# Kernel optimization log

Hardware: AMD Instinct MI355X
Metric: run time of the kernel (lower is better)

## Reference

```python
import jax, jax.numpy as jnp
import numpy as np

N_QUBITS = 8
N_LAYERS = 3
BATCH = 8192


def setup_inputs() -> dict:
    key = jax.random.key(0)
    k0, k1, k2, k3 = jax.random.split(key, 4)
    return {
        "x": jax.random.normal(k0, (BATCH, N_QUBITS), jnp.float32),
        "quantum_weights": jax.random.normal(k1, (N_LAYERS, N_QUBITS, 2), jnp.float32) * 0.1,
        "W1": jax.random.normal(k2, (N_QUBITS, 64), jnp.float32) / np.float32(np.sqrt(N_QUBITS)),
        "b1": jnp.zeros((64,), jnp.float32),
        "W2": jax.random.normal(k3, (64, 256), jnp.float32) / np.float32(np.sqrt(64)),
        "b2": jnp.zeros((256,), jnp.float32),
    }


def _ry(theta):
    # RY(t) = [[cos t/2, -sin t/2], [sin t/2, cos t/2]]; theta: [] or [B]
    c = jnp.cos(theta * 0.5)
    s = jnp.sin(theta * 0.5)
    U = jnp.stack([jnp.stack([c, -s], axis=-1), jnp.stack([s, c], axis=-1)], axis=-2)
    return U.astype(jnp.complex64)


def _rz(theta):
    # RZ(t) = diag(e^{-it/2}, e^{it/2})
    em = jnp.exp(-0.5j * theta.astype(jnp.complex64))
    ep = jnp.exp(0.5j * theta.astype(jnp.complex64))
    z = jnp.zeros_like(em)
    return jnp.stack([jnp.stack([em, z], axis=-1), jnp.stack([z, ep], axis=-1)], axis=-2)


def _apply_1q(state, U, q):
    # state: [B, 2,2,...,2]; qubit q lives on axis q+1. U: [2,2] (shared) or [B,2,2].
    s = jnp.moveaxis(state, q + 1, -1)
    if U.ndim == 3:
        s = jnp.einsum('b...i,bji->b...j', s, U)
    else:
        s = jnp.einsum('b...i,ji->b...j', s, U)
    return jnp.moveaxis(s, -1, q + 1)


def _cnot(state, c, t):
    # flip target bit on the control=1 slice
    s = jnp.moveaxis(state, (c + 1, t + 1), (1, 2))
    s = jnp.stack([s[:, 0], s[:, 1, ::-1]], axis=1)
    return jnp.moveaxis(s, (1, 2), (c + 1, t + 1))


def _quantum_forward(x, qw):
    B = x.shape[0]
    xmin = x.min(axis=1, keepdims=True)
    xmax = x.max(axis=1, keepdims=True)
    xn = (x - xmin) / (xmax - xmin + 1e-8)
    # |0...0> state, shape [B, 2]*n
    state = jnp.zeros((B,) + (2,) * N_QUBITS, jnp.complex64)
    state = state.at[(slice(None),) + (0,) * N_QUBITS].set(1.0)
    # feature encoding: RY(x_norm * pi), per-sample angles
    for q in range(N_QUBITS):
        state = _apply_1q(state, _ry(xn[:, q] * jnp.pi), q)
    # variational layers
    for layer in range(N_LAYERS):
        for q in range(N_QUBITS):
            state = _apply_1q(state, _ry(qw[layer, q, 0]), q)
            state = _apply_1q(state, _rz(qw[layer, q, 1]), q)
        for q in range(N_QUBITS):
            state = _cnot(state, q, (q + 1) % N_QUBITS)
    probs = jnp.real(state * jnp.conj(state))  # [B, 2]*n, float32
    z = []
    for q in range(N_QUBITS):
        p = probs.sum(axis=tuple(a for a in range(1, N_QUBITS + 1) if a != q + 1))
        z.append(p[:, 0] - p[:, 1])  # <Z_q>
    return jnp.stack(z, axis=1)  # [B, n_qubits]


def reference(x, quantum_weights, W1, b1, W2, b2):
    z = _quantum_forward(x, quantum_weights).astype(jnp.float32)
    h = jax.nn.relu(z @ W1 + b1)
    return h @ W2 + b2
```

## Files before the change

### kernel.cpp

```cpp
#include <hip/hip_runtime.h>

#define NQ 8
#define NLAYERS 3

typedef unsigned int uint2ev __attribute__((ext_vector_type(2)));

template<int MASK>
__device__ __forceinline__ float xorlane(float v, int r) {
    if constexpr (MASK == 1) {
        return __int_as_float(__builtin_amdgcn_mov_dpp(__float_as_int(v), 0xB1, 0xF, 0xF, false));
    } else if constexpr (MASK == 2) {
        return __int_as_float(__builtin_amdgcn_mov_dpp(__float_as_int(v), 0x4E, 0xF, 0xF, false));
    } else if constexpr (MASK == 4) {
        float a = __int_as_float(__builtin_amdgcn_update_dpp(0, __float_as_int(v), 0x114, 0xF, 0xF, false));
        float b = __int_as_float(__builtin_amdgcn_update_dpp(0, __float_as_int(v), 0x104, 0xF, 0xF, false));
        return (r & 4) ? a : b;
    } else if constexpr (MASK == 8) {
        return __int_as_float(__builtin_amdgcn_mov_dpp(__float_as_int(v), 0x128, 0xF, 0xF, false));
    }
}

template<int CTRL>
__device__ __forceinline__ float dpp_add_stage(float v) {
    int moved = __builtin_amdgcn_update_dpp(0, __float_as_int(v), CTRL, 0xF, 0xF, false);
    return v + __int_as_float(moved);
}
__device__ __forceinline__ float rowsum15(float v) {
    v = dpp_add_stage<0x111>(v);
    v = dpp_add_stage<0x112>(v);
    v = dpp_add_stage<0x114>(v);
    v = dpp_add_stage<0x118>(v);
    return v;
}

__device__ __forceinline__ void ry_pair(float c, float s, float& a0, float& a1) {
    float n0 = c * a0 - s * a1;
    float n1 = s * a0 + c * a1;
    a0 = n0; a1 = n1;
}

__device__ __forceinline__ void rz_amp(float cp, float ssp, float& re, float& im) {
    float nr = re * cp - im * ssp;
    float ni = im * cp + re * ssp;
    re = nr; im = ni;
}

template<int Q>
__device__ __forceinline__ void ry16(float c, float s, float ar[16], float ai[16], int r) {
    if constexpr (Q < 4) {
        constexpr int M = 1 << Q;
#pragma unroll
        for (int j = 0; j < 16; ++j) if (!(j & M)) {
            ry_pair(c, s, ar[j], ar[j | M]);
            ry_pair(c, s, ai[j], ai[j | M]);
        }
    } else {
        constexpr int LM = 1 << (Q - 4);
        float sgn = (r & LM) ? s : -s;
#pragma unroll
        for (int j = 0; j < 16; ++j) {
            float pr = xorlane<LM>(ar[j], r);
            float pi = xorlane<LM>(ai[j], r);
            ar[j] = c * ar[j] + sgn * pr;
            ai[j] = c * ai[j] + sgn * pi;
        }
    }
}

template<int Q>
__device__ __forceinline__ void rz16(float cp, float sp, float ar[16], float ai[16], int r) {
    if constexpr (Q < 4) {
#pragma unroll
        for (int j = 0; j < 16; ++j) {
            float ssp = ((j >> Q) & 1) ? sp : -sp;
            rz_amp(cp, ssp, ar[j], ai[j]);
        }
    } else {
        float ssp = (r & (1 << (Q - 4))) ? sp : -sp;
#pragma unroll
        for (int j = 0; j < 16; ++j) rz_amp(cp, ssp, ar[j], ai[j]);
    }
}

#define SWAP2(a, b) { float _t = a; a = b; b = _t; }

__device__ __forceinline__ void ring16(float ar[16], float ai[16], int r) {
    SWAP2(ar[1], ar[3]);  SWAP2(ai[1], ai[3]);
    SWAP2(ar[5], ar[7]);  SWAP2(ai[5], ai[7]);
    SWAP2(ar[9], ar[11]); SWAP2(ai[9], ai[11]);
    SWAP2(ar[13], ar[15]); SWAP2(ai[13], ai[15]);
    SWAP2(ar[2], ar[6]);  SWAP2(ai[2], ai[6]);
    SWAP2(ar[3], ar[7]);  SWAP2(ai[3], ai[7]);
    SWAP2(ar[10], ar[14]); SWAP2(ai[10], ai[14]);
    SWAP2(ar[11], ar[15]); SWAP2(ai[11], ai[15]);
    SWAP2(ar[4], ar[12]); SWAP2(ai[4], ai[12]);
    SWAP2(ar[5], ar[13]); SWAP2(ai[5], ai[13]);
    SWAP2(ar[6], ar[14]); SWAP2(ai[6], ai[14]);
    SWAP2(ar[7], ar[15]); SWAP2(ai[7], ai[15]);
#pragma unroll
    for (int j = 8; j < 16; ++j) {
        ar[j] = xorlane<1>(ar[j], r);
        ai[j] = xorlane<1>(ai[j], r);
    }
    {
        bool hi = (r & 1) != 0;
#pragma unroll
        for (int j = 0; j < 16; ++j) {
            float pr = xorlane<2>(ar[j], r);
            float pi = xorlane<2>(ai[j], r);
            ar[j] = hi ? pr : ar[j];
            ai[j] = hi ? pi : ai[j];
        }
    }
    {
        bool hi = (r & 2) != 0;
#pragma unroll
        for (int j = 0; j < 16; ++j) {
            float pr = xorlane<4>(ar[j], r);
            float pi = xorlane<4>(ai[j], r);
            ar[j] = hi ? pr : ar[j];
            ai[j] = hi ? pi : ai[j];
        }
    }
    {
        bool hi = (r & 4) != 0;
#pragma unroll
        for (int j = 0; j < 16; ++j) {
            float pr = xorlane<8>(ar[j], r);
            float pi = xorlane<8>(ai[j], r);
            ar[j] = hi ? pr : ar[j];
            ai[j] = hi ? pi : ai[j];
        }
    }
    {
        bool hi = (r & 8) != 0;
#pragma unroll
        for (int j = 0; j < 16; j += 2) {
            float t0r = ar[j], t1r = ar[j + 1];
            ar[j]     = hi ? t1r : t0r;
            ar[j + 1] = hi ? t0r : t1r;
            float t0i = ai[j], t1i = ai[j + 1];
            ai[j]     = hi ? t1i : t0i;
            ai[j + 1] = hi ? t0i : t1i;
        }
    }
}

#define CMUL(rr, ri, xr, xi, yr, yi) { float _tr = (xr)*(yr) - (xi)*(yi); \
                                       float _ti = (xr)*(yi) + (xi)*(yr); \
                                       rr = _tr; ri = _ti; }

__global__ __launch_bounds__(256) void qfused(
    const float* __restrict__ x,
    const float* __restrict__ qw,
    const float* __restrict__ W1,
    const float* __restrict__ b1,
    const float* __restrict__ W2,
    const float* __restrict__ b2,
    float* __restrict__ out,
    int B)
{
    __shared__ float4 tab[NLAYERS * NQ];
    __shared__ float z_lds[16][8];
    __shared__ float h_lds[16][64];

    int tid = threadIdx.x;
    if (tid < NLAYERS * NQ) {
        float w0 = 0.5f * qw[tid * 2 + 0];
        float w1 = 0.5f * qw[tid * 2 + 1];
        if (tid < 8)
            tab[tid] = make_float4(w0, 0.f, __cosf(w1), __sinf(w1));
        else
            tab[tid] = make_float4(__cosf(w0), __sinf(w0), __cosf(w1), __sinf(w1));
    }
    __syncthreads();

    int lane = tid & 63;
    int wid  = tid >> 6;
    int g    = lane >> 4;
    int r    = lane & 15;
    int sl   = wid * 4 + g;
    int sbase = blockIdx.x * 16;
    int sample = sbase + sl;
    if (sample >= B) sample = B - 1;

    const float4* x4 = (const float4*)(x + sample * 8);
    float4 xa = x4[0], xb = x4[1];
    float xs[8] = {xa.x, xa.y, xa.z, xa.w, xb.x, xb.y, xb.z, xb.w};
    float xmin = xs[0], xmax = xs[0];
#pragma unroll
    for (int q = 1; q < 8; ++q) {
        xmin = fminf(xmin, xs[q]);
        xmax = fmaxf(xmax, xs[q]);
    }
    float inv_pi2 = 1.5707963267948966f / (xmax - xmin + 1e-8f);

    float cc[8], ss[8], cw[8], sw[8];
#pragma unroll
    for (int q = 0; q < 8; ++q) {
        float4 t0 = tab[q];
        float a = fmaf(xs[q] - xmin, inv_pi2, t0.x);
        cc[q] = __cosf(a);
        ss[q] = __sinf(a);
        cw[q] = t0.z;
        sw[q] = t0.w;
    }

    int r0v = r & 1, r3v = (r >> 3) & 1;

    float X0r[2], X0i[2], X1r[2], X1i[2], X2r[2], X2i[2], X3r[2], X3i[2], X4r[2], X4i[2];
#pragma unroll
    for (int k = 0; k < 2; ++k) {
        { int b = k ^ r3v; float rr = b ? ss[0] : cc[0];
          X0r[k] = rr * cw[0]; X0i[k] = (b ? rr : -rr) * sw[0]; }
        { int b = k ^ r3v; float rr = b ? ss[1] : cc[1];
          X1r[k] = rr * cw[1]; X1i[k] = (b ? rr : -rr) * sw[1]; }
        { int b = k;        float rr = b ? ss[2] : cc[2];
          X2r[k] = rr * cw[2]; X2i[k] = (b ? rr : -rr) * sw[2]; }
        { int b = k;        float rr = b ? ss[3] : cc[3];
          X3r[k] = rr * cw[3]; X3i[k] = (b ? rr : -rr) * sw[3]; }
        { int b = k ^ r0v;  float rr = b ? ss[4] : cc[4];
          X4r[k] = rr * cw[4]; X4i[k] = (b ? rr : -rr) * sw[4]; }
    }

    float plr, pli;
    {
        int b5 = (r ^ (r >> 1)) & 1;
        int b6 = ((r >> 1) ^ (r >> 2)) & 1;
        int b7 = ((r >> 2) ^ (r >> 3)) & 1;
        float r5 = b5 ? ss[5] : cc[5];
        float f5r = r5 * cw[5], f5i = (b5 ? r5 : -r5) * sw[5];
        float r6 = b6 ? ss[6] : cc[6];
        float f6r = r6 * cw[6], f6i = (b6 ? r6 : -r6) * sw[6];
        float r7 = b7 ? ss[7] : cc[7];
        float f7r = r7 * cw[7], f7i = (b7 ? r7 : -r7) * sw[7];
        CMUL(plr, pli, f5r, f5i, f6r, f6i);
        CMUL(plr, pli, plr, pli, f7r, f7i);
    }

    float PPr[2][2], PPi[2][2];
    {
        float t0r, t0i, t1r, t1i;
        CMUL(t0r, t0i, plr, pli, X0r[0], X0i[0]);
        CMUL(t1r, t1i, plr, pli, X0r[1], X0i[1]);
        CMUL(PPr[0][0], PPi[0][0], t0r, t0i, X1r[0], X1i[0]);
        CMUL(PPr[0][1], PPi[0][1], t0r, t0i, X1r[1], X1i[1]);
        CMUL(PPr[1][0], PPi[1][0], t1r, t1i, X1r[1], X1i[1]);
        CMUL(PPr[1][1], PPi[1][1], t1r, t1i, X1r[0], X1i[0]);
    }
    float Qr[2][2], Qi[2][2];
    CMUL(Qr[0][0], Qi[0][0], X3r[0], X3i[0], X4r[0], X4i[0]);
    CMUL(Qr[0][1], Qi[0][1], X3r[1], X3i[1], X4r[1], X4i[1]);
    CMUL(Qr[1][0], Qi[1][0], X3r[1], X3i[1], X4r[0], X4i[0]);
    CMUL(Qr[1][1], Qi[1][1], X3r[0], X3i[0], X4r[1], X4i[1]);
    float Rr[2][2][2], Ri[2][2][2];
#pragma unroll
    for (int j1 = 0; j1 < 2; ++j1)
#pragma unroll
        for (int j2 = 0; j2 < 2; ++j2)
#pragma unroll
            for (int j3 = 0; j3 < 2; ++j3) {
                int k = j1 ^ j2;
                CMUL(Rr[j1][j2][j3], Ri[j1][j2][j3], X2r[k], X2i[k], Qr[j2][j3], Qi[j2][j3]);
            }

    float ar[16], ai[16];
#pragma unroll
    for (int j3 = 0; j3 < 2; ++j3)
#pragma unroll
        for (int j2 = 0; j2 < 2; ++j2)
#pragma unroll
            for (int j1 = 0; j1 < 2; ++j1)
#pragma unroll
                for (int j0 = 0; j0 < 2; ++j0) {
                    int j = j0 + 2 * j1 + 4 * j2 + 8 * j3;
                    CMUL(ar[j], ai[j], PPr[j0][j1], PPi[j0][j1], Rr[j1][j2][j3], Ri[j1][j2][j3]);
                }

    {
        float4 t;
        t = tab[8];  ry16<0>(t.x, t.y, ar, ai, r); rz16<0>(t.z, t.w, ar, ai, r);
        t = tab[9];  ry16<1>(t.x, t.y, ar, ai, r); rz16<1>(t.z, t.w, ar, ai, r);
        t = tab[10]; ry16<2>(t.x, t.y, ar, ai, r); rz16<2>(t.z, t.w, ar, ai, r);
        t = tab[11]; ry16<3>(t.x, t.y, ar, ai, r); rz16<3>(t.z, t.w, ar, ai, r);
        t = tab[12]; ry16<4>(t.x, t.y, ar, ai, r); rz16<4>(t.z, t.w, ar, ai, r);
        t = tab[13]; ry16<5>(t.x, t.y, ar, ai, r); rz16<5>(t.z, t.w, ar, ai, r);
        t = tab[14]; ry16<6>(t.x, t.y, ar, ai, r); rz16<6>(t.z, t.w, ar, ai, r);
        t = tab[15]; ry16<7>(t.x, t.y, ar, ai, r); rz16<7>(t.z, t.w, ar, ai, r);
    }
    ring16(ar, ai, r);
    {
        float4 t;
        t = tab[16]; ry16<0>(t.x, t.y, ar, ai, r);
        t = tab[17]; ry16<1>(t.x, t.y, ar, ai, r);
        t = tab[18]; ry16<2>(t.x, t.y, ar, ai, r);
        t = tab[19]; ry16<3>(t.x, t.y, ar, ai, r);
        t = tab[20]; ry16<4>(t.x, t.y, ar, ai, r);
        t = tab[21]; ry16<5>(t.x, t.y, ar, ai, r);
        t = tab[22]; ry16<6>(t.x, t.y, ar, ai, r);
        t = tab[23]; ry16<7>(t.x, t.y, ar, ai, r);
    }

    float P[16];
#pragma unroll
    for (int j = 0; j < 16; ++j) P[j] = ar[j] * ar[j] + ai[j] * ai[j];

    float Sp[8], Dp[8];
#pragma unroll
    for (int k = 0; k < 8; ++k) {
        Sp[k] = P[2 * k] + P[2 * k + 1];
        Dp[k] = P[2 * k] - P[2 * k + 1];
    }
    float U0 = ((Sp[0] - Sp[1]) - (Sp[2] - Sp[3])) - ((Sp[4] - Sp[5]) - (Sp[6] - Sp[7]));
    float U3 = ((Dp[0] - Dp[1]) - (Dp[2] - Dp[3])) - ((Dp[4] - Dp[5]) - (Dp[6] - Dp[7]));
    float U1 = (Dp[0] - Dp[1]) + (Dp[2] - Dp[3]) + (Dp[4] - Dp[5]) + (Dp[6] - Dp[7]);
    float U2 = ((Dp[0] - Dp[1]) - (Dp[2] - Dp[3])) + ((Dp[4] - Dp[5]) - (Dp[6] - Dp[7]));

    int p1 = r & 1;
    int p2 = (r ^ (r >> 1)) & 1;
    int p3 = (r ^ (r >> 1) ^ (r >> 2)) & 1;
    int p4 = (r ^ (r >> 1) ^ (r >> 2) ^ (r >> 3)) & 1;

    float z0 = rowsum15(p4 ? -U0 : U0);
    float z1 = rowsum15(U1);
    float z2 = rowsum15(U2);
    float z3 = rowsum15(U3);
    float z4 = rowsum15(p1 ? -U3 : U3);
    float z5 = rowsum15(p2 ? -U3 : U3);
    float z6 = rowsum15(p3 ? -U3 : U3);
    float z7 = rowsum15(p4 ? -U3 : U3);

    if (r == 15) {
        *(float4*)&z_lds[sl][0] = make_float4(z0, z1, z2, z3);
        *(float4*)&z_lds[sl][4] = make_float4(z4, z5, z6, z7);
    }
    __syncthreads();

    {
        int s_l = tid >> 4;
        int i_l = (tid & 15) * 4;
        float4 za = *(const float4*)&z_lds[s_l][0];
        float4 zb = *(const float4*)&z_lds[s_l][4];
        float zq[8] = {za.x, za.y, za.z, za.w, zb.x, zb.y, zb.z, zb.w};
        float4 acc = *(const float4*)(b1 + i_l);
#pragma unroll
        for (int q = 0; q < 8; ++q) {
            float4 w = *(const float4*)(W1 + q * 64 + i_l);
            acc.x += zq[q] * w.x; acc.y += zq[q] * w.y;
            acc.z += zq[q] * w.z; acc.w += zq[q] * w.w;
        }
        acc.x = fmaxf(acc.x, 0.f); acc.y = fmaxf(acc.y, 0.f);
        acc.z = fmaxf(acc.z, 0.f); acc.w = fmaxf(acc.w, 0.f);
        *(float4*)&h_lds[s_l][i_l] = acc;
    }
    __syncthreads();

    int sg = tid >> 6;
    int c4 = (tid & 63) * 4;
    float4 bb = *(const float4*)(b2 + c4);
    float4 a0 = bb, a1 = bb, a2 = bb, a3 = bb;
    const int sO = sg * 4;

#pragma unroll 2
    for (int i4 = 0; i4 < 16; ++i4) {
        const float* wrow = W2 + i4 * 4 * 256 + c4;
        float4 w0 = *(const float4*)(wrow);
        float4 w1 = *(const float4*)(wrow + 256);
        float4 w2 = *(const float4*)(wrow + 512);
        float4 w3 = *(const float4*)(wrow + 768);
        float4 h0 = *(const float4*)&h_lds[sO + 0][i4 * 4];
        float4 h1 = *(const float4*)&h_lds[sO + 1][i4 * 4];
        float4 h2 = *(const float4*)&h_lds[sO + 2][i4 * 4];
        float4 h3 = *(const float4*)&h_lds[sO + 3][i4 * 4];

        a0.x += h0.x*w0.x + h0.y*w1.x + h0.z*w2.x + h0.w*w3.x;
        a0.y += h0.x*w0.y + h0.y*w1.y + h0.z*w2.y + h0.w*w3.y;
        a0.z += h0.x*w0.z + h0.y*w1.z + h0.z*w2.z + h0.w*w3.z;
        a0.w += h0.x*w0.w + h0.y*w1.w + h0.z*w2.w + h0.w*w3.w;

        a1.x += h1.x*w0.x + h1.y*w1.x + h1.z*w2.x + h1.w*w3.x;
        a1.y += h1.x*w0.y + h1.y*w1.y + h1.z*w2.y + h1.w*w3.y;
        a1.z += h1.x*w0.z + h1.y*w1.z + h1.z*w2.z + h1.w*w3.z;
        a1.w += h1.x*w0.w + h1.y*w1.w + h1.z*w2.w + h1.w*w3.w;

        a2.x += h2.x*w0.x + h2.y*w1.x + h2.z*w2.x + h2.w*w3.x;
        a2.y += h2.x*w0.y + h2.y*w1.y + h2.z*w2.y + h2.w*w3.y;
        a2.z += h2.x*w0.z + h2.y*w1.z + h2.z*w2.z + h2.w*w3.z;
        a2.w += h2.x*w0.w + h2.y*w1.w + h2.z*w2.w + h2.w*w3.w;

        a3.x += h3.x*w0.x + h3.y*w1.x + h3.z*w2.x + h3.w*w3.x;
        a3.y += h3.x*w0.y + h3.y*w1.y + h3.z*w2.y + h3.w*w3.y;
        a3.z += h3.x*w0.z + h3.y*w1.z + h3.z*w2.z + h3.w*w3.z;
        a3.w += h3.x*w0.w + h3.y*w1.w + h3.z*w2.w + h3.w*w3.w;
    }

    int srow = sbase + sO;
    if (srow + 0 < B) *(float4*)(out + (srow + 0) * 256 + c4) = a0;
    if (srow + 1 < B) *(float4*)(out + (srow + 1) * 256 + c4) = a1;
    if (srow + 2 < B) *(float4*)(out + (srow + 2) * 256 + c4) = a2;
    if (srow + 3 < B) *(float4*)(out + (srow + 3) * 256 + c4) = a3;
}

extern "C" void kernel_launch(void* const* d_in, const int* in_sizes, int n_in,
                              void* d_out, int out_size, void* d_ws, size_t ws_size,
                              hipStream_t stream) {
    const float* x  = (const float*)d_in[0];
    const float* qw = (const float*)d_in[1];
    const float* W1 = (const float*)d_in[2];
    const float* b1 = (const float*)d_in[3];
    const float* W2 = (const float*)d_in[4];
    const float* b2 = (const float*)d_in[5];
    float* out = (float*)d_out;

    int B = in_sizes[0] / NQ;

    qfused<<<(B + 15) / 16, 256, 0, stream>>>(x, qw, W1, b1, W2, b2, out, B);
}
```

Before: 21.72 us.

## Spread each sample's state vector over 32 lanes instead of 16

```diff
diff --git a/kernel.cpp b/kernel.cpp
--- a/kernel.cpp
+++ b/kernel.cpp
@@ -17,6 +17,9 @@
         return (r & 4) ? a : b;
     } else if constexpr (MASK == 8) {
         return __int_as_float(__builtin_amdgcn_mov_dpp(__float_as_int(v), 0x128, 0xF, 0xF, false));
+    } else if constexpr (MASK == 16) {
+        uint2ev rr = __builtin_amdgcn_permlane16_swap(__float_as_uint(v), __float_as_uint(v), false, false);
+        return __uint_as_float((r & 16) ? rr.x : rr.y);
     }
 }
 
@@ -25,11 +28,12 @@
     int moved = __builtin_amdgcn_update_dpp(0, __float_as_int(v), CTRL, 0xF, 0xF, false);
     return v + __int_as_float(moved);
 }
-__device__ __forceinline__ float rowsum15(float v) {
+__device__ __forceinline__ float halfsum31(float v) {
     v = dpp_add_stage<0x111>(v);
     v = dpp_add_stage<0x112>(v);
     v = dpp_add_stage<0x114>(v);
     v = dpp_add_stage<0x118>(v);
+    v = dpp_add_stage<0x142>(v);
     return v;
 }
 
@@ -46,19 +50,19 @@
 }
 
 template<int Q>
-__device__ __forceinline__ void ry16(float c, float s, float ar[16], float ai[16], int r) {
-    if constexpr (Q < 4) {
+__device__ __forceinline__ void ry8(float c, float s, float ar[8], float ai[8], int r) {
+    if constexpr (Q < 3) {
         constexpr int M = 1 << Q;
 #pragma unroll
-        for (int j = 0; j < 16; ++j) if (!(j & M)) {
+        for (int j = 0; j < 8; ++j) if (!(j & M)) {
             ry_pair(c, s, ar[j], ar[j | M]);
             ry_pair(c, s, ai[j], ai[j | M]);
         }
     } else {
-        constexpr int LM = 1 << (Q - 4);
+        constexpr int LM = 1 << (Q - 3);
         float sgn = (r & LM) ? s : -s;
 #pragma unroll
-        for (int j = 0; j < 16; ++j) {
+        for (int j = 0; j < 8; ++j) {
             float pr = xorlane<LM>(ar[j], r);
             float pi = xorlane<LM>(ai[j], r);
             ar[j] = c * ar[j] + sgn * pr;
@@ -68,44 +72,36 @@
 }
 
 template<int Q>
-__device__ __forceinline__ void rz16(float cp, float sp, float ar[16], float ai[16], int r) {
-    if constexpr (Q < 4) {
-#pragma unroll
-        for (int j = 0; j < 16; ++j) {
+__device__ __forceinline__ void rz8(float cp, float sp, float ar[8], float ai[8], int r) {
+    if constexpr (Q < 3) {
+#pragma unroll
+        for (int j = 0; j < 8; ++j) {
             float ssp = ((j >> Q) & 1) ? sp : -sp;
             rz_amp(cp, ssp, ar[j], ai[j]);
         }
     } else {
-        float ssp = (r & (1 << (Q - 4))) ? sp : -sp;
-#pragma unroll
-        for (int j = 0; j < 16; ++j) rz_amp(cp, ssp, ar[j], ai[j]);
+        float ssp = (r & (1 << (Q - 3))) ? sp : -sp;
+#pragma unroll
+        for (int j = 0; j < 8; ++j) rz_amp(cp, ssp, ar[j], ai[j]);
     }
 }
 
 #define SWAP2(a, b) { float _t = a; a = b; b = _t; }
 
-__device__ __forceinline__ void ring16(float ar[16], float ai[16], int r) {
-    SWAP2(ar[1], ar[3]);  SWAP2(ai[1], ai[3]);
-    SWAP2(ar[5], ar[7]);  SWAP2(ai[5], ai[7]);
-    SWAP2(ar[9], ar[11]); SWAP2(ai[9], ai[11]);
-    SWAP2(ar[13], ar[15]); SWAP2(ai[13], ai[15]);
-    SWAP2(ar[2], ar[6]);  SWAP2(ai[2], ai[6]);
-    SWAP2(ar[3], ar[7]);  SWAP2(ai[3], ai[7]);
-    SWAP2(ar[10], ar[14]); SWAP2(ai[10], ai[14]);
-    SWAP2(ar[11], ar[15]); SWAP2(ai[11], ai[15]);
-    SWAP2(ar[4], ar[12]); SWAP2(ai[4], ai[12]);
-    SWAP2(ar[5], ar[13]); SWAP2(ai[5], ai[13]);
-    SWAP2(ar[6], ar[14]); SWAP2(ai[6], ai[14]);
-    SWAP2(ar[7], ar[15]); SWAP2(ai[7], ai[15]);
-#pragma unroll
-    for (int j = 8; j < 16; ++j) {
+__device__ __forceinline__ void ring8(float ar[8], float ai[8], int r) {
+    SWAP2(ar[1], ar[3]); SWAP2(ai[1], ai[3]);
+    SWAP2(ar[5], ar[7]); SWAP2(ai[5], ai[7]);
+    SWAP2(ar[2], ar[6]); SWAP2(ai[2], ai[6]);
+    SWAP2(ar[3], ar[7]); SWAP2(ai[3], ai[7]);
+#pragma unroll
+    for (int j = 4; j < 8; ++j) {
         ar[j] = xorlane<1>(ar[j], r);
         ai[j] = xorlane<1>(ai[j], r);
     }
     {
         bool hi = (r & 1) != 0;
 #pragma unroll
-        for (int j = 0; j < 16; ++j) {
+        for (int j = 0; j < 8; ++j) {
             float pr = xorlane<2>(ar[j], r);
             float pi = xorlane<2>(ai[j], r);
             ar[j] = hi ? pr : ar[j];
@@ -115,7 +111,7 @@
     {
         bool hi = (r & 2) != 0;
 #pragma unroll
-        for (int j = 0; j < 16; ++j) {
+        for (int j = 0; j < 8; ++j) {
             float pr = xorlane<4>(ar[j], r);
             float pi = xorlane<4>(ai[j], r);
             ar[j] = hi ? pr : ar[j];
@@ -125,7 +121,7 @@
     {
         bool hi = (r & 4) != 0;
 #pragma unroll
-        for (int j = 0; j < 16; ++j) {
+        for (int j = 0; j < 8; ++j) {
             float pr = xorlane<8>(ar[j], r);
             float pi = xorlane<8>(ai[j], r);
             ar[j] = hi ? pr : ar[j];
@@ -135,7 +131,17 @@
     {
         bool hi = (r & 8) != 0;
 #pragma unroll
-        for (int j = 0; j < 16; j += 2) {
+        for (int j = 0; j < 8; ++j) {
+            float pr = xorlane<16>(ar[j], r);
+            float pi = xorlane<16>(ai[j], r);
+            ar[j] = hi ? pr : ar[j];
+            ai[j] = hi ? pi : ai[j];
+        }
+    }
+    {
+        bool hi = (r & 16) != 0;
+#pragma unroll
+        for (int j = 0; j < 8; j += 2) {
             float t0r = ar[j], t1r = ar[j + 1];
             ar[j]     = hi ? t1r : t0r;
             ar[j + 1] = hi ? t0r : t1r;
@@ -161,8 +167,8 @@
     int B)
 {
     __shared__ float4 tab[NLAYERS * NQ];
-    __shared__ float z_lds[16][8];
-    __shared__ float h_lds[16][64];
+    __shared__ float z_lds[8][8];
+    __shared__ float h_lds[8][64];
 
     int tid = threadIdx.x;
     if (tid < NLAYERS * NQ) {
@@ -177,10 +183,10 @@
 
     int lane = tid & 63;
     int wid  = tid >> 6;
-    int g    = lane >> 4;
-    int r    = lane & 15;
-    int sl   = wid * 4 + g;
-    int sbase = blockIdx.x * 16;
+    int g    = lane >> 5;
+    int r    = lane & 31;
+    int sl   = wid * 2 + g;
+    int sbase = blockIdx.x * 8;
     int sample = sbase + sl;
     if (sample >= B) sample = B - 1;
 
@@ -200,166 +206,150 @@
     for (int q = 0; q < 8; ++q) {
         float4 t0 = tab[q];
         float a = fmaf(xs[q] - xmin, inv_pi2, t0.x);
-        cc[q] = __cosf(a);
-        ss[q] = __sinf(a);
+        __sincosf(a, &ss[q], &cc[q]);
         cw[q] = t0.z;
         sw[q] = t0.w;
     }
 
-    int r0v = r & 1, r3v = (r >> 3) & 1;
-
-    float X0r[2], X0i[2], X1r[2], X1i[2], X2r[2], X2i[2], X3r[2], X3i[2], X4r[2], X4i[2];
+    int u4 = (r >> 4) & 1;
+    int w0v = r & 1;
+
+    float X0r[2], X0i[2], X1r[2], X1i[2], X2r[2], X2i[2], X3r[2], X3i[2];
 #pragma unroll
     for (int k = 0; k < 2; ++k) {
-        { int b = k ^ r3v; float rr = b ? ss[0] : cc[0];
+        { int b = k ^ u4;  float rr = b ? ss[0] : cc[0];
           X0r[k] = rr * cw[0]; X0i[k] = (b ? rr : -rr) * sw[0]; }
-        { int b = k ^ r3v; float rr = b ? ss[1] : cc[1];
+        { int b = k ^ u4;  float rr = b ? ss[1] : cc[1];
           X1r[k] = rr * cw[1]; X1i[k] = (b ? rr : -rr) * sw[1]; }
-        { int b = k;        float rr = b ? ss[2] : cc[2];
+        { int b = k;       float rr = b ? ss[2] : cc[2];
           X2r[k] = rr * cw[2]; X2i[k] = (b ? rr : -rr) * sw[2]; }
-        { int b = k;        float rr = b ? ss[3] : cc[3];
+        { int b = k ^ w0v; float rr = b ? ss[3] : cc[3];
           X3r[k] = rr * cw[3]; X3i[k] = (b ? rr : -rr) * sw[3]; }
-        { int b = k ^ r0v;  float rr = b ? ss[4] : cc[4];
-          X4r[k] = rr * cw[4]; X4i[k] = (b ? rr : -rr) * sw[4]; }
     }
 
     float plr, pli;
     {
-        int b5 = (r ^ (r >> 1)) & 1;
-        int b6 = ((r >> 1) ^ (r >> 2)) & 1;
-        int b7 = ((r >> 2) ^ (r >> 3)) & 1;
-        float r5 = b5 ? ss[5] : cc[5];
-        float f5r = r5 * cw[5], f5i = (b5 ? r5 : -r5) * sw[5];
-        float r6 = b6 ? ss[6] : cc[6];
-        float f6r = r6 * cw[6], f6i = (b6 ? r6 : -r6) * sw[6];
-        float r7 = b7 ? ss[7] : cc[7];
-        float f7r = r7 * cw[7], f7i = (b7 ? r7 : -r7) * sw[7];
-        CMUL(plr, pli, f5r, f5i, f6r, f6i);
+        int b4 = (r ^ (r >> 1)) & 1;
+        int b5 = ((r >> 1) ^ (r >> 2)) & 1;
+        int b6 = ((r >> 2) ^ (r >> 3)) & 1;
+        int b7 = ((r >> 3) ^ (r >> 4)) & 1;
+        float r4_ = b4 ? ss[4] : cc[4];
+        float f4r = r4_ * cw[4], f4i = (b4 ? r4_ : -r4_) * sw[4];
+        float r5_ = b5 ? ss[5] : cc[5];
+        float f5r = r5_ * cw[5], f5i = (b5 ? r5_ : -r5_) * sw[5];
+        float r6_ = b6 ? ss[6] : cc[6];
+        float f6r = r6_ * cw[6], f6i = (b6 ? r6_ : -r6_) * sw[6];
+        float r7_ = b7 ? ss[7] : cc[7];
+        float f7r = r7_ * cw[7], f7i = (b7 ? r7_ : -r7_) * sw[7];
+        CMUL(plr, pli, f4r, f4i, f5r, f5i);
+        CMUL(plr, pli, plr, pli, f6r, f6i);
         CMUL(plr, pli, plr, pli, f7r, f7i);
     }
 
-    float PPr[2][2], PPi[2][2];
+    float PTr[2][2], PTi[2][2];
     {
         float t0r, t0i, t1r, t1i;
         CMUL(t0r, t0i, plr, pli, X0r[0], X0i[0]);
         CMUL(t1r, t1i, plr, pli, X0r[1], X0i[1]);
-        CMUL(PPr[0][0], PPi[0][0], t0r, t0i, X1r[0], X1i[0]);
-        CMUL(PPr[0][1], PPi[0][1], t0r, t0i, X1r[1], X1i[1]);
-        CMUL(PPr[1][0], PPi[1][0], t1r, t1i, X1r[1], X1i[1]);
-        CMUL(PPr[1][1], PPi[1][1], t1r, t1i, X1r[0], X1i[0]);
-    }
-    float Qr[2][2], Qi[2][2];
-    CMUL(Qr[0][0], Qi[0][0], X3r[0], X3i[0], X4r[0], X4i[0]);
-    CMUL(Qr[0][1], Qi[0][1], X3r[1], X3i[1], X4r[1], X4i[1]);
-    CMUL(Qr[1][0], Qi[1][0], X3r[1], X3i[1], X4r[0], X4i[0]);
-    CMUL(Qr[1][1], Qi[1][1], X3r[0], X3i[0], X4r[1], X4i[1]);
-    float Rr[2][2][2], Ri[2][2][2];
-#pragma unroll
-    for (int j1 = 0; j1 < 2; ++j1)
-#pragma unroll
-        for (int j2 = 0; j2 < 2; ++j2)
-#pragma unroll
-            for (int j3 = 0; j3 < 2; ++j3) {
-                int k = j1 ^ j2;
-                CMUL(Rr[j1][j2][j3], Ri[j1][j2][j3], X2r[k], X2i[k], Qr[j2][j3], Qi[j2][j3]);
+        CMUL(PTr[0][0], PTi[0][0], t0r, t0i, X1r[0], X1i[0]);
+        CMUL(PTr[0][1], PTi[0][1], t0r, t0i, X1r[1], X1i[1]);
+        CMUL(PTr[1][0], PTi[1][0], t1r, t1i, X1r[1], X1i[1]);
+        CMUL(PTr[1][1], PTi[1][1], t1r, t1i, X1r[0], X1i[0]);
+    }
+    float Sr[2][2], Si[2][2];
+    CMUL(Sr[0][0], Si[0][0], X2r[0], X2i[0], X3r[0], X3i[0]);
+    CMUL(Sr[0][1], Si[0][1], X2r[1], X2i[1], X3r[1], X3i[1]);
+    CMUL(Sr[1][0], Si[1][0], X2r[1], X2i[1], X3r[0], X3i[0]);
+    CMUL(Sr[1][1], Si[1][1], X2r[0], X2i[0], X3r[1], X3i[1]);
+
+    float ar[8], ai[8];
+#pragma unroll
+    for (int j2 = 0; j2 < 2; ++j2)
+#pragma unroll
+        for (int j1 = 0; j1 < 2; ++j1)
+#pragma unroll
+            for (int j0 = 0; j0 < 2; ++j0) {
+                int j = j0 + 2 * j1 + 4 * j2;
+                CMUL(ar[j], ai[j], PTr[j0][j1], PTi[j0][j1], Sr[j1][j2], Si[j1][j2]);
             }
 
-    float ar[16], ai[16];
-#pragma unroll
-    for (int j3 = 0; j3 < 2; ++j3)
-#pragma unroll
-        for (int j2 = 0; j2 < 2; ++j2)
-#pragma unroll
-            for (int j1 = 0; j1 < 2; ++j1)
-#pragma unroll
-                for (int j0 = 0; j0 < 2; ++j0) {
-                    int j = j0 + 2 * j1 + 4 * j2 + 8 * j3;
-                    CMUL(ar[j], ai[j], PPr[j0][j1], PPi[j0][j1], Rr[j1][j2][j3], Ri[j1][j2][j3]);
-                }
-
     {
         float4 t;
-        t = tab[8];  ry16<0>(t.x, t.y, ar, ai, r); rz16<0>(t.z, t.w, ar, ai, r);
-        t = tab[9];  ry16<1>(t.x, t.y, ar, ai, r); rz16<1>(t.z, t.w, ar, ai, r);
-        t = tab[10]; ry16<2>(t.x, t.y, ar, ai, r); rz16<2>(t.z, t.w, ar, ai, r);
-        t = tab[11]; ry16<3>(t.x, t.y, ar, ai, r); rz16<3>(t.z, t.w, ar, ai, r);
-        t = tab[12]; ry16<4>(t.x, t.y, ar, ai, r); rz16<4>(t.z, t.w, ar, ai, r);
-        t = tab[13]; ry16<5>(t.x, t.y, ar, ai, r); rz16<5>(t.z, t.w, ar, ai, r);
-        t = tab[14]; ry16<6>(t.x, t.y, ar, ai, r); rz16<6>(t.z, t.w, ar, ai, r);
-        t = tab[15]; ry16<7>(t.x, t.y, ar, ai, r); rz16<7>(t.z, t.w, ar, ai, r);
-    }
-    ring16(ar, ai, r);
+        t = tab[8];  ry8<0>(t.x, t.y, ar, ai, r); rz8<0>(t.z, t.w, ar, ai, r);
+        t = tab[9];  ry8<1>(t.x, t.y, ar, ai, r); rz8<1>(t.z, t.w, ar, ai, r);
+        t = tab[10]; ry8<2>(t.x, t.y, ar, ai, r); rz8<2>(t.z, t.w, ar, ai, r);
+        t = tab[11]; ry8<3>(t.x, t.y, ar, ai, r); rz8<3>(t.z, t.w, ar, ai, r);
+        t = tab[12]; ry8<4>(t.x, t.y, ar, ai, r); rz8<4>(t.z, t.w, ar, ai, r);
+        t = tab[13]; ry8<5>(t.x, t.y, ar, ai, r); rz8<5>(t.z, t.w, ar, ai, r);
+        t = tab[14]; ry8<6>(t.x, t.y, ar, ai, r); rz8<6>(t.z, t.w, ar, ai, r);
+        t = tab[15]; ry8<7>(t.x, t.y, ar, ai, r); rz8<7>(t.z, t.w, ar, ai, r);
+    }
+    ring8(ar, ai, r);
     {
         float4 t;
-        t = tab[16]; ry16<0>(t.x, t.y, ar, ai, r);
-        t = tab[17]; ry16<1>(t.x, t.y, ar, ai, r);
-        t = tab[18]; ry16<2>(t.x, t.y, ar, ai, r);
-        t = tab[19]; ry16<3>(t.x, t.y, ar, ai, r);
-        t = tab[20]; ry16<4>(t.x, t.y, ar, ai, r);
-        t = tab[21]; ry16<5>(t.x, t.y, ar, ai, r);
-        t = tab[22]; ry16<6>(t.x, t.y, ar, ai, r);
-        t = tab[23]; ry16<7>(t.x, t.y, ar, ai, r);
-    }
-
-    float P[16];
-#pragma unroll
-    for (int j = 0; j < 16; ++j) P[j] = ar[j] * ar[j] + ai[j] * ai[j];
-
-    float Sp[8], Dp[8];
-#pragma unroll
-    for (int k = 0; k < 8; ++k) {
-        Sp[k] = P[2 * k] + P[2 * k + 1];
-        Dp[k] = P[2 * k] - P[2 * k + 1];
-    }
-    float U0 = ((Sp[0] - Sp[1]) - (Sp[2] - Sp[3])) - ((Sp[4] - Sp[5]) - (Sp[6] - Sp[7]));
-    float U3 = ((Dp[0] - Dp[1]) - (Dp[2] - Dp[3])) - ((Dp[4] - Dp[5]) - (Dp[6] - Dp[7]));
-    float U1 = (Dp[0] - Dp[1]) + (Dp[2] - Dp[3]) + (Dp[4] - Dp[5]) + (Dp[6] - Dp[7]);
-    float U2 = ((Dp[0] - Dp[1]) - (Dp[2] - Dp[3])) + ((Dp[4] - Dp[5]) - (Dp[6] - Dp[7]));
-
-    int p1 = r & 1;
-    int p2 = (r ^ (r >> 1)) & 1;
-    int p3 = (r ^ (r >> 1) ^ (r >> 2)) & 1;
-    int p4 = (r ^ (r >> 1) ^ (r >> 2) ^ (r >> 3)) & 1;
-
-    float z0 = rowsum15(p4 ? -U0 : U0);
-    float z1 = rowsum15(U1);
-    float z2 = rowsum15(U2);
-    float z3 = rowsum15(U3);
-    float z4 = rowsum15(p1 ? -U3 : U3);
-    float z5 = rowsum15(p2 ? -U3 : U3);
-    float z6 = rowsum15(p3 ? -U3 : U3);
-    float z7 = rowsum15(p4 ? -U3 : U3);
-
-    if (r == 15) {
+        t = tab[16]; ry8<0>(t.x, t.y, ar, ai, r);
+        t = tab[17]; ry8<1>(t.x, t.y, ar, ai, r);
+        t = tab[18]; ry8<2>(t.x, t.y, ar, ai, r);
+        t = tab[19]; ry8<3>(t.x, t.y, ar, ai, r);
+        t = tab[20]; ry8<4>(t.x, t.y, ar, ai, r);
+        t = tab[21]; ry8<5>(t.x, t.y, ar, ai, r);
+        t = tab[22]; ry8<6>(t.x, t.y, ar, ai, r);
+        t = tab[23]; ry8<7>(t.x, t.y, ar, ai, r);
+    }
+
+    float P[8];
+#pragma unroll
+    for (int j = 0; j < 8; ++j) P[j] = ar[j] * ar[j] + ai[j] * ai[j];
+
+    float G01  = (P[0] - P[1] - P[2] + P[3]) + (P[4] - P[5] - P[6] + P[7]);
+    float G012 = (P[0] - P[1] - P[2] + P[3]) - (P[4] - P[5] - P[6] + P[7]);
+    float G12  = (P[0] + P[1] - P[2] - P[3]) - (P[4] + P[5] - P[6] - P[7]);
+
+    int pr1 = r & 1;
+    int pr2 = (r ^ (r >> 1)) & 1;
+    int pr3 = (r ^ (r >> 1) ^ (r >> 2)) & 1;
+    int pr4 = (r ^ (r >> 1) ^ (r >> 2) ^ (r >> 3)) & 1;
+    int pr5 = (r ^ (r >> 1) ^ (r >> 2) ^ (r >> 3) ^ (r >> 4)) & 1;
+
+    float z0 = halfsum31(pr5 ? -G12  : G12);
+    float z1 = halfsum31(G01);
+    float z2 = halfsum31(G012);
+    float z3 = halfsum31(pr1 ? -G012 : G012);
+    float z4 = halfsum31(pr2 ? -G012 : G012);
+    float z5 = halfsum31(pr3 ? -G012 : G012);
+    float z6 = halfsum31(pr4 ? -G012 : G012);
+    float z7 = halfsum31(pr5 ? -G012 : G012);
+
+    if (r == 31) {
         *(float4*)&z_lds[sl][0] = make_float4(z0, z1, z2, z3);
         *(float4*)&z_lds[sl][4] = make_float4(z4, z5, z6, z7);
     }
     __syncthreads();
 
     {
-        int s_l = tid >> 4;
-        int i_l = (tid & 15) * 4;
+        int s_l = tid >> 5;
+        int i_l = (tid & 31) * 2;
         float4 za = *(const float4*)&z_lds[s_l][0];
         float4 zb = *(const float4*)&z_lds[s_l][4];
         float zq[8] = {za.x, za.y, za.z, za.w, zb.x, zb.y, zb.z, zb.w};
-        float4 acc = *(const float4*)(b1 + i_l);
+        float2 acc = *(const float2*)(b1 + i_l);
 #pragma unroll
         for (int q = 0; q < 8; ++q) {
-            float4 w = *(const float4*)(W1 + q * 64 + i_l);
-            acc.x += zq[q] * w.x; acc.y += zq[q] * w.y;
-            acc.z += zq[q] * w.z; acc.w += zq[q] * w.w;
-        }
-        acc.x = fmaxf(acc.x, 0.f); acc.y = fmaxf(acc.y, 0.f);
-        acc.z = fmaxf(acc.z, 0.f); acc.w = fmaxf(acc.w, 0.f);
-        *(float4*)&h_lds[s_l][i_l] = acc;
+            float2 w = *(const float2*)(W1 + q * 64 + i_l);
+            acc.x += zq[q] * w.x;
+            acc.y += zq[q] * w.y;
+        }
+        acc.x = fmaxf(acc.x, 0.f);
+        acc.y = fmaxf(acc.y, 0.f);
+        *(float2*)&h_lds[s_l][i_l] = acc;
     }
     __syncthreads();
 
     int sg = tid >> 6;
     int c4 = (tid & 63) * 4;
     float4 bb = *(const float4*)(b2 + c4);
-    float4 a0 = bb, a1 = bb, a2 = bb, a3 = bb;
-    const int sO = sg * 4;
+    float4 a0 = bb, a1 = bb;
+    const int sO = sg * 2;
 
 #pragma unroll 2
     for (int i4 = 0; i4 < 16; ++i4) {
@@ -370,8 +360,6 @@
         float4 w3 = *(const float4*)(wrow + 768);
         float4 h0 = *(const float4*)&h_lds[sO + 0][i4 * 4];
         float4 h1 = *(const float4*)&h_lds[sO + 1][i4 * 4];
-        float4 h2 = *(const float4*)&h_lds[sO + 2][i4 * 4];
-        float4 h3 = *(const float4*)&h_lds[sO + 3][i4 * 4];
 
         a0.x += h0.x*w0.x + h0.y*w1.x + h0.z*w2.x + h0.w*w3.x;
         a0.y += h0.x*w0.y + h0.y*w1.y + h0.z*w2.y + h0.w*w3.y;
@@ -382,23 +370,11 @@
         a1.y += h1.x*w0.y + h1.y*w1.y + h1.z*w2.y + h1.w*w3.y;
         a1.z += h1.x*w0.z + h1.y*w1.z + h1.z*w2.z + h1.w*w3.z;
         a1.w += h1.x*w0.w + h1.y*w1.w + h1.z*w2.w + h1.w*w3.w;
-
-        a2.x += h2.x*w0.x + h2.y*w1.x + h2.z*w2.x + h2.w*w3.x;
-        a2.y += h2.x*w0.y + h2.y*w1.y + h2.z*w2.y + h2.w*w3.y;
-        a2.z += h2.x*w0.z + h2.y*w1.z + h2.z*w2.z + h2.w*w3.z;
-        a2.w += h2.x*w0.w + h2.y*w1.w + h2.z*w2.w + h2.w*w3.w;
-
-        a3.x += h3.x*w0.x + h3.y*w1.x + h3.z*w2.x + h3.w*w3.x;
-        a3.y += h3.x*w0.y + h3.y*w1.y + h3.z*w2.y + h3.w*w3.y;
-        a3.z += h3.x*w0.z + h3.y*w1.z + h3.z*w2.z + h3.w*w3.z;
-        a3.w += h3.x*w0.w + h3.y*w1.w + h3.z*w2.w + h3.w*w3.w;
     }
 
     int srow = sbase + sO;
     if (srow + 0 < B) *(float4*)(out + (srow + 0) * 256 + c4) = a0;
     if (srow + 1 < B) *(float4*)(out + (srow + 1) * 256 + c4) = a1;
-    if (srow + 2 < B) *(float4*)(out + (srow + 2) * 256 + c4) = a2;
-    if (srow + 3 < B) *(float4*)(out + (srow + 3) * 256 + c4) = a3;
 }
 
 extern "C" void kernel_launch(void* const* d_in, const int* in_sizes, int n_in,
@@ -414,5 +390,5 @@
 
     int B = in_sizes[0] / NQ;
 
-    qfused<<<(B + 15) / 16, 256, 0, stream>>>(x, qw, W1, b1, W2, b2, out, B);
-}
+    qfused<<<(B + 7) / 8, 256, 0, stream>>>(x, qw, W1, b1, W2, b2, out, B);
+}
```

After: 24.17 us. +11.3%, slower.

## Pack complex amplitudes into float2 vectors and merge layer-2 RZ gates into one diagonal

Applied to the files above, without the earlier changes.

```diff
diff --git a/kernel.cpp b/kernel.cpp
--- a/kernel.cpp
+++ b/kernel.cpp
@@ -4,6 +4,7 @@
 #define NLAYERS 3
 
 typedef unsigned int uint2ev __attribute__((ext_vector_type(2)));
+typedef float f2 __attribute__((ext_vector_type(2)));
 
 template<int MASK>
 __device__ __forceinline__ float xorlane(float v, int r) {
@@ -20,6 +21,14 @@
     }
 }
 
+template<int MASK>
+__device__ __forceinline__ f2 xorlane2(f2 v, int r) {
+    f2 o;
+    o.x = xorlane<MASK>(v.x, r);
+    o.y = xorlane<MASK>(v.y, r);
+    return o;
+}
+
 template<int CTRL>
 __device__ __forceinline__ float dpp_add_stage(float v) {
     int moved = __builtin_amdgcn_update_dpp(0, __float_as_int(v), CTRL, 0xF, 0xF, false);
@@ -33,122 +42,94 @@
     return v;
 }
 
-__device__ __forceinline__ void ry_pair(float c, float s, float& a0, float& a1) {
-    float n0 = c * a0 - s * a1;
-    float n1 = s * a0 + c * a1;
-    a0 = n0; a1 = n1;
-}
-
-__device__ __forceinline__ void rz_amp(float cp, float ssp, float& re, float& im) {
-    float nr = re * cp - im * ssp;
-    float ni = im * cp + re * ssp;
-    re = nr; im = ni;
+__device__ __forceinline__ f2 cmul(f2 a, f2 b) {
+    f2 r;
+    r.x = a.x * b.x - a.y * b.y;
+    r.y = a.x * b.y + a.y * b.x;
+    return r;
+}
+
+__device__ __forceinline__ f2 splat(float c) { f2 v; v.x = c; v.y = c; return v; }
+
+__device__ __forceinline__ f2 sel2(bool hi, f2 a, f2 b) {
+    f2 o;
+    o.x = hi ? a.x : b.x;
+    o.y = hi ? a.y : b.y;
+    return o;
 }
 
 template<int Q>
-__device__ __forceinline__ void ry16(float c, float s, float ar[16], float ai[16], int r) {
+__device__ __forceinline__ void ry16(float c, float s, f2 A[16], int r) {
+    f2 vc = splat(c), vs = splat(s);
     if constexpr (Q < 4) {
         constexpr int M = 1 << Q;
 #pragma unroll
         for (int j = 0; j < 16; ++j) if (!(j & M)) {
-            ry_pair(c, s, ar[j], ar[j | M]);
-            ry_pair(c, s, ai[j], ai[j | M]);
+            f2 a0 = A[j], a1 = A[j | M];
+            A[j]     = vc * a0 - vs * a1;
+            A[j | M] = vs * a0 + vc * a1;
         }
     } else {
         constexpr int LM = 1 << (Q - 4);
-        float sgn = (r & LM) ? s : -s;
+        f2 vsg = (r & LM) ? vs : (splat(0.f) - vs);
 #pragma unroll
         for (int j = 0; j < 16; ++j) {
-            float pr = xorlane<LM>(ar[j], r);
-            float pi = xorlane<LM>(ai[j], r);
-            ar[j] = c * ar[j] + sgn * pr;
-            ai[j] = c * ai[j] + sgn * pi;
-        }
-    }
-}
-
-template<int Q>
-__device__ __forceinline__ void rz16(float cp, float sp, float ar[16], float ai[16], int r) {
-    if constexpr (Q < 4) {
+            f2 p = xorlane2<LM>(A[j], r);
+            A[j] = vc * A[j] + vsg * p;
+        }
+    }
+}
+
+__device__ __forceinline__ void ring16(f2 A[16], int r) {
+    f2 t;
+    t = A[1]; A[1] = A[3]; A[3] = t;
+    t = A[5]; A[5] = A[7]; A[7] = t;
+    t = A[9]; A[9] = A[11]; A[11] = t;
+    t = A[13]; A[13] = A[15]; A[15] = t;
+    t = A[2]; A[2] = A[6]; A[6] = t;
+    t = A[3]; A[3] = A[7]; A[7] = t;
+    t = A[10]; A[10] = A[14]; A[14] = t;
+    t = A[11]; A[11] = A[15]; A[15] = t;
+    t = A[4]; A[4] = A[12]; A[12] = t;
+    t = A[5]; A[5] = A[13]; A[13] = t;
+    t = A[6]; A[6] = A[14]; A[14] = t;
+    t = A[7]; A[7] = A[15]; A[15] = t;
+#pragma unroll
+    for (int j = 8; j < 16; ++j) A[j] = xorlane2<1>(A[j], r);
+    {
+        bool hi = (r & 1) != 0;
 #pragma unroll
         for (int j = 0; j < 16; ++j) {
-            float ssp = ((j >> Q) & 1) ? sp : -sp;
-            rz_amp(cp, ssp, ar[j], ai[j]);
-        }
-    } else {
-        float ssp = (r & (1 << (Q - 4))) ? sp : -sp;
-#pragma unroll
-        for (int j = 0; j < 16; ++j) rz_amp(cp, ssp, ar[j], ai[j]);
-    }
-}
-
-#define SWAP2(a, b) { float _t = a; a = b; b = _t; }
-
-__device__ __forceinline__ void ring16(float ar[16], float ai[16], int r) {
-    SWAP2(ar[1], ar[3]);  SWAP2(ai[1], ai[3]);
-    SWAP2(ar[5], ar[7]);  SWAP2(ai[5], ai[7]);
-    SWAP2(ar[9], ar[11]); SWAP2(ai[9], ai[11]);
-    SWAP2(ar[13], ar[15]); SWAP2(ai[13], ai[15]);
-    SWAP2(ar[2], ar[6]);  SWAP2(ai[2], ai[6]);
-    SWAP2(ar[3], ar[7]);  SWAP2(ai[3], ai[7]);
-    SWAP2(ar[10], ar[14]); SWAP2(ai[10], ai[14]);
-    SWAP2(ar[11], ar[15]); SWAP2(ai[11], ai[15]);
-    SWAP2(ar[4], ar[12]); SWAP2(ai[4], ai[12]);
-    SWAP2(ar[5], ar[13]); SWAP2(ai[5], ai[13]);
-    SWAP2(ar[6], ar[14]); SWAP2(ai[6], ai[14]);
-    SWAP2(ar[7], ar[15]); SWAP2(ai[7], ai[15]);
-#pragma unroll
-    for (int j = 8; j < 16; ++j) {
-        ar[j] = xorlane<1>(ar[j], r);
-        ai[j] = xorlane<1>(ai[j], r);
-    }
-    {
-        bool hi = (r & 1) != 0;
+            f2 p = xorlane2<2>(A[j], r);
+            A[j] = sel2(hi, p, A[j]);
+        }
+    }
+    {
+        bool hi = (r & 2) != 0;
 #pragma unroll
         for (int j = 0; j < 16; ++j) {
-            float pr = xorlane<2>(ar[j], r);
-            float pi = xorlane<2>(ai[j], r);
-            ar[j] = hi ? pr : ar[j];
-            ai[j] = hi ? pi : ai[j];
-        }
-    }
-    {
-        bool hi = (r & 2) != 0;
+            f2 p = xorlane2<4>(A[j], r);
+            A[j] = sel2(hi, p, A[j]);
+        }
+    }
+    {
+        bool hi = (r & 4) != 0;
 #pragma unroll
         for (int j = 0; j < 16; ++j) {
-            float pr = xorlane<4>(ar[j], r);
-            float pi = xorlane<4>(ai[j], r);
-            ar[j] = hi ? pr : ar[j];
-            ai[j] = hi ? pi : ai[j];
-        }
-    }
-    {
-        bool hi = (r & 4) != 0;
-#pragma unroll
-        for (int j = 0; j < 16; ++j) {
-            float pr = xorlane<8>(ar[j], r);
-            float pi = xorlane<8>(ai[j], r);
-            ar[j] = hi ? pr : ar[j];
-            ai[j] = hi ? pi : ai[j];
+            f2 p = xorlane2<8>(A[j], r);
+            A[j] = sel2(hi, p, A[j]);
         }
     }
     {
         bool hi = (r & 8) != 0;
 #pragma unroll
         for (int j = 0; j < 16; j += 2) {
-            float t0r = ar[j], t1r = ar[j + 1];
-            ar[j]     = hi ? t1r : t0r;
-            ar[j + 1] = hi ? t0r : t1r;
-            float t0i = ai[j], t1i = ai[j + 1];
-            ai[j]     = hi ? t1i : t0i;
-            ai[j + 1] = hi ? t0i : t1i;
-        }
-    }
-}
-
-#define CMUL(rr, ri, xr, xi, yr, yi) { float _tr = (xr)*(yr) - (xi)*(yi); \
-                                       float _ti = (xr)*(yi) + (xi)*(yr); \
-                                       rr = _tr; ri = _ti; }
+            f2 t0 = A[j], t1 = A[j + 1];
+            A[j]     = sel2(hi, t1, t0);
+            A[j + 1] = sel2(hi, t0, t1);
+        }
+    }
+}
 
 __global__ __launch_bounds__(256) void qfused(
     const float* __restrict__ x,
@@ -200,71 +181,67 @@
     for (int q = 0; q < 8; ++q) {
         float4 t0 = tab[q];
         float a = fmaf(xs[q] - xmin, inv_pi2, t0.x);
-        cc[q] = __cosf(a);
-        ss[q] = __sinf(a);
+        __sincosf(a, &ss[q], &cc[q]);
         cw[q] = t0.z;
         sw[q] = t0.w;
     }
 
     int r0v = r & 1, r3v = (r >> 3) & 1;
 
-    float X0r[2], X0i[2], X1r[2], X1i[2], X2r[2], X2i[2], X3r[2], X3i[2], X4r[2], X4i[2];
+    f2 X0[2], X1[2], X2[2], X3[2], X4[2];
 #pragma unroll
     for (int k = 0; k < 2; ++k) {
         { int b = k ^ r3v; float rr = b ? ss[0] : cc[0];
-          X0r[k] = rr * cw[0]; X0i[k] = (b ? rr : -rr) * sw[0]; }
+          X0[k].x = rr * cw[0]; X0[k].y = (b ? rr : -rr) * sw[0]; }
         { int b = k ^ r3v; float rr = b ? ss[1] : cc[1];
-          X1r[k] = rr * cw[1]; X1i[k] = (b ? rr : -rr) * sw[1]; }
+          X1[k].x = rr * cw[1]; X1[k].y = (b ? rr : -rr) * sw[1]; }
         { int b = k;        float rr = b ? ss[2] : cc[2];
-          X2r[k] = rr * cw[2]; X2i[k] = (b ? rr : -rr) * sw[2]; }
+          X2[k].x = rr * cw[2]; X2[k].y = (b ? rr : -rr) * sw[2]; }
         { int b = k;        float rr = b ? ss[3] : cc[3];
-          X3r[k] = rr * cw[3]; X3i[k] = (b ? rr : -rr) * sw[3]; }
+          X3[k].x = rr * cw[3]; X3[k].y = (b ? rr : -rr) * sw[3]; }
         { int b = k ^ r0v;  float rr = b ? ss[4] : cc[4];
-          X4r[k] = rr * cw[4]; X4i[k] = (b ? rr : -rr) * sw[4]; }
-    }
-
-    float plr, pli;
+          X4[k].x = rr * cw[4]; X4[k].y = (b ? rr : -rr) * sw[4]; }
+    }
+
+    f2 pl;
     {
         int b5 = (r ^ (r >> 1)) & 1;
         int b6 = ((r >> 1) ^ (r >> 2)) & 1;
         int b7 = ((r >> 2) ^ (r >> 3)) & 1;
+        f2 f5, f6, f7;
         float r5 = b5 ? ss[5] : cc[5];
-        float f5r = r5 * cw[5], f5i = (b5 ? r5 : -r5) * sw[5];
+        f5.x = r5 * cw[5]; f5.y = (b5 ? r5 : -r5) * sw[5];
         float r6 = b6 ? ss[6] : cc[6];
-        float f6r = r6 * cw[6], f6i = (b6 ? r6 : -r6) * sw[6];
+        f6.x = r6 * cw[6]; f6.y = (b6 ? r6 : -r6) * sw[6];
         float r7 = b7 ? ss[7] : cc[7];
-        float f7r = r7 * cw[7], f7i = (b7 ? r7 : -r7) * sw[7];
-        CMUL(plr, pli, f5r, f5i, f6r, f6i);
-        CMUL(plr, pli, plr, pli, f7r, f7i);
-    }
-
-    float PPr[2][2], PPi[2][2];
-    {
-        float t0r, t0i, t1r, t1i;
-        CMUL(t0r, t0i, plr, pli, X0r[0], X0i[0]);
-        CMUL(t1r, t1i, plr, pli, X0r[1], X0i[1]);
-        CMUL(PPr[0][0], PPi[0][0], t0r, t0i, X1r[0], X1i[0]);
-        CMUL(PPr[0][1], PPi[0][1], t0r, t0i, X1r[1], X1i[1]);
-        CMUL(PPr[1][0], PPi[1][0], t1r, t1i, X1r[1], X1i[1]);
-        CMUL(PPr[1][1], PPi[1][1], t1r, t1i, X1r[0], X1i[0]);
-    }
-    float Qr[2][2], Qi[2][2];
-    CMUL(Qr[0][0], Qi[0][0], X3r[0], X3i[0], X4r[0], X4i[0]);
-    CMUL(Qr[0][1], Qi[0][1], X3r[1], X3i[1], X4r[1], X4i[1]);
-    CMUL(Qr[1][0], Qi[1][0], X3r[1], X3i[1], X4r[0], X4i[0]);
-    CMUL(Qr[1][1], Qi[1][1], X3r[0], X3i[0], X4r[1], X4i[1]);
-    float Rr[2][2][2], Ri[2][2][2];
+        f7.x = r7 * cw[7]; f7.y = (b7 ? r7 : -r7) * sw[7];
+        pl = cmul(cmul(f5, f6), f7);
+    }
+
+    f2 PP[2][2];
+    {
+        f2 t0 = cmul(pl, X0[0]);
+        f2 t1 = cmul(pl, X0[1]);
+        PP[0][0] = cmul(t0, X1[0]);
+        PP[0][1] = cmul(t0, X1[1]);
+        PP[1][0] = cmul(t1, X1[1]);
+        PP[1][1] = cmul(t1, X1[0]);
+    }
+    f2 Q34[2][2];
+    Q34[0][0] = cmul(X3[0], X4[0]);
+    Q34[0][1] = cmul(X3[1], X4[1]);
+    Q34[1][0] = cmul(X3[1], X4[0]);
+    Q34[1][1] = cmul(X3[0], X4[1]);
+    f2 R[2][2][2];
 #pragma unroll
     for (int j1 = 0; j1 < 2; ++j1)
 #pragma unroll
         for (int j2 = 0; j2 < 2; ++j2)
 #pragma unroll
-            for (int j3 = 0; j3 < 2; ++j3) {
-                int k = j1 ^ j2;
-                CMUL(Rr[j1][j2][j3], Ri[j1][j2][j3], X2r[k], X2i[k], Qr[j2][j3], Qi[j2][j3]);
-            }
-
-    float ar[16], ai[16];
+            for (int j3 = 0; j3 < 2; ++j3)
+                R[j1][j2][j3] = cmul(X2[j1 ^ j2], Q34[j2][j3]);
+
+    f2 A[16];
 #pragma unroll
     for (int j3 = 0; j3 < 2; ++j3)
 #pragma unroll
@@ -274,36 +251,77 @@
 #pragma unroll
                 for (int j0 = 0; j0 < 2; ++j0) {
                     int j = j0 + 2 * j1 + 4 * j2 + 8 * j3;
-                    CMUL(ar[j], ai[j], PPr[j0][j1], PPi[j0][j1], Rr[j1][j2][j3], Ri[j1][j2][j3]);
+                    A[j] = cmul(PP[j0][j1], R[j1][j2][j3]);
                 }
 
     {
         float4 t;
-        t = tab[8];  ry16<0>(t.x, t.y, ar, ai, r); rz16<0>(t.z, t.w, ar, ai, r);
-        t = tab[9];  ry16<1>(t.x, t.y, ar, ai, r); rz16<1>(t.z, t.w, ar, ai, r);
-        t = tab[10]; ry16<2>(t.x, t.y, ar, ai, r); rz16<2>(t.z, t.w, ar, ai, r);
-        t = tab[11]; ry16<3>(t.x, t.y, ar, ai, r); rz16<3>(t.z, t.w, ar, ai, r);
-        t = tab[12]; ry16<4>(t.x, t.y, ar, ai, r); rz16<4>(t.z, t.w, ar, ai, r);
-        t = tab[13]; ry16<5>(t.x, t.y, ar, ai, r); rz16<5>(t.z, t.w, ar, ai, r);
-        t = tab[14]; ry16<6>(t.x, t.y, ar, ai, r); rz16<6>(t.z, t.w, ar, ai, r);
-        t = tab[15]; ry16<7>(t.x, t.y, ar, ai, r); rz16<7>(t.z, t.w, ar, ai, r);
-    }
-    ring16(ar, ai, r);
+        t = tab[8];  ry16<0>(t.x, t.y, A, r);
+        t = tab[9];  ry16<1>(t.x, t.y, A, r);
+        t = tab[10]; ry16<2>(t.x, t.y, A, r);
+        t = tab[11]; ry16<3>(t.x, t.y, A, r);
+        t = tab[12]; ry16<4>(t.x, t.y, A, r);
+        t = tab[13]; ry16<5>(t.x, t.y, A, r);
+        t = tab[14]; ry16<6>(t.x, t.y, A, r);
+        t = tab[15]; ry16<7>(t.x, t.y, A, r);
+    }
+
+    {
+        f2 L;
+        {
+            float4 t4 = tab[12], t5 = tab[13], t6 = tab[14], t7 = tab[15];
+            f2 d4, d5, d6, d7;
+            d4.x = t4.z; d4.y = (r & 1) ? t4.w : -t4.w;
+            d5.x = t5.z; d5.y = (r & 2) ? t5.w : -t5.w;
+            d6.x = t6.z; d6.y = (r & 4) ? t6.w : -t6.w;
+            d7.x = t7.z; d7.y = (r & 8) ? t7.w : -t7.w;
+            L = cmul(cmul(d4, d5), cmul(d6, d7));
+        }
+        float4 t0q = tab[8], t1q = tab[9], t2q = tab[10], t3q = tab[11];
+        f2 d0n, d0p, d1n, d1p, d2n, d2p, d3n, d3p;
+        d0n.x = t0q.z; d0n.y = -t0q.w;  d0p.x = t0q.z; d0p.y = t0q.w;
+        d1n.x = t1q.z; d1n.y = -t1q.w;  d1p.x = t1q.z; d1p.y = t1q.w;
+        d2n.x = t2q.z; d2n.y = -t2q.w;  d2p.x = t2q.z; d2p.y = t2q.w;
+        d3n.x = t3q.z; d3n.y = -t3q.w;  d3p.x = t3q.z; d3p.y = t3q.w;
+
+        f2 t01[4];
+        {
+            f2 l0 = cmul(L, d0n), l1 = cmul(L, d0p);
+            t01[0] = cmul(l0, d1n);
+            t01[1] = cmul(l1, d1n);
+            t01[2] = cmul(l0, d1p);
+            t01[3] = cmul(l1, d1p);
+        }
+        f2 m23[4];
+        m23[0] = cmul(d2n, d3n);
+        m23[1] = cmul(d2p, d3n);
+        m23[2] = cmul(d2n, d3p);
+        m23[3] = cmul(d2p, d3p);
+
+#pragma unroll
+        for (int j = 0; j < 16; ++j) {
+            f2 D = cmul(t01[j & 3], m23[j >> 2]);
+            A[j] = cmul(A[j], D);
+        }
+    }
+
+    ring16(A, r);
+
     {
         float4 t;
-        t = tab[16]; ry16<0>(t.x, t.y, ar, ai, r);
-        t = tab[17]; ry16<1>(t.x, t.y, ar, ai, r);
-        t = tab[18]; ry16<2>(t.x, t.y, ar, ai, r);
-        t = tab[19]; ry16<3>(t.x, t.y, ar, ai, r);
-        t = tab[20]; ry16<4>(t.x, t.y, ar, ai, r);
-        t = tab[21]; ry16<5>(t.x, t.y, ar, ai, r);
-        t = tab[22]; ry16<6>(t.x, t.y, ar, ai, r);
-        t = tab[23]; ry16<7>(t.x, t.y, ar, ai, r);
+        t = tab[16]; ry16<0>(t.x, t.y, A, r);
+        t = tab[17]; ry16<1>(t.x, t.y, A, r);
+        t = tab[18]; ry16<2>(t.x, t.y, A, r);
+        t = tab[19]; ry16<3>(t.x, t.y, A, r);
+        t = tab[20]; ry16<4>(t.x, t.y, A, r);
+        t = tab[21]; ry16<5>(t.x, t.y, A, r);
+        t = tab[22]; ry16<6>(t.x, t.y, A, r);
+        t = tab[23]; ry16<7>(t.x, t.y, A, r);
     }
 
     float P[16];
 #pragma unroll
-    for (int j = 0; j < 16; ++j) P[j] = ar[j] * ar[j] + ai[j] * ai[j];
+    for (int j = 0; j < 16; ++j) P[j] = A[j].x * A[j].x + A[j].y * A[j].y;
 
     float Sp[8], Dp[8];
 #pragma unroll
```

Measured after the change: 20.10 us. -7.4%, faster.
